# Performance work log

Hardware: AMD Instinct MI355X
Metric: run time of the kernel (lower is better)

Reference implementation:

```python
import jax, jax.numpy as jnp
import numpy as np

E = 8        # num_experts
K = 2        # top_k routing
D = 1024     # d_model
F = 4096     # expert hidden (ffn) dim
EPS = 1e-5


def _layernorm(h, g, b):
    # h: [E, T, C]; g, b: [E, C]
    mu = h.mean(axis=-1, keepdims=True)
    var = ((h - mu) ** 2).mean(axis=-1, keepdims=True)
    return (h - mu) * jax.lax.rsqrt(var + EPS) * g[:, None, :] + b[:, None, :]


def setup_inputs() -> dict:
    key = jax.random.key(0)
    ks = jax.random.split(key, 8)
    B, S = 2, 2048
    x = jax.random.normal(ks[0], (B, S, D), dtype=jnp.float32)
    Wr = jax.random.normal(ks[1], (D, E), dtype=jnp.float32) / np.sqrt(D)
    br = jnp.zeros((E,), dtype=jnp.float32)
    W1 = jax.random.normal(ks[2], (E, D, F), dtype=jnp.float32) / np.sqrt(D)
    b1 = jnp.zeros((E, F), dtype=jnp.float32)
    g1 = jnp.ones((E, F), dtype=jnp.float32)
    be1 = jnp.zeros((E, F), dtype=jnp.float32)
    W2 = jax.random.normal(ks[3], (E, F, D), dtype=jnp.float32) / np.sqrt(F)
    b2 = jnp.zeros((E, D), dtype=jnp.float32)
    g2 = jnp.ones((E, D), dtype=jnp.float32)
    be2 = jnp.zeros((E, D), dtype=jnp.float32)
    return {"x": x, "Wr": Wr, "br": br, "W1": W1, "b1": b1, "g1": g1,
            "be1": be1, "W2": W2, "b2": b2, "g2": g2, "be2": be2}


def reference(x, Wr, br, W1, b1, g1, be1, W2, b2, g2, be2):
    B, S, _ = x.shape
    xt = x.reshape(-1, D)                       # [T, D] token matrix
    # --- router + sampler: top-k softmax probs, renormalized over the k slots
    logits = xt @ Wr + br                       # [T, E]
    p = jax.nn.softmax(logits, axis=-1)
    probs, idx = jax.lax.top_k(p, K)            # [T, K]
    probs = probs / probs.sum(axis=-1, keepdims=True)
    # --- experts layer 1: Linear -> relu -> LayerNorm, per expert
    h = jnp.einsum('td,edf->etf', xt, W1) + b1[:, None, :]   # [E, T, F]
    h = _layernorm(jax.nn.relu(h), g1, be1)
    # --- experts layer 2: Linear -> relu -> LayerNorm
    y = jnp.einsum('etf,efd->etd', h, W2) + b2[:, None, :]   # [E, T, D]
    y = _layernorm(jax.nn.relu(y), g2, be2)
    # --- weighted scatter-combine: gate[t,e] = sum_k 1[idx[t,k]==e] * probs[t,k]
    gate = (jax.nn.one_hot(idx, E, dtype=x.dtype) * probs[..., None]).sum(axis=1)  # [T, E]
    out = jnp.einsum('te,etd->td', gate, y)     # index_add combine, dense form
    return out.reshape(B, S, D)
```

## Files before the change

kernel.cpp:

```cpp
#include <hip/hip_runtime.h>


#define E_N 8
#define TOPK 2
#define DM 1024
#define FF 4096
#define NTOK 4096
#define NA 8192
#define LN_EPS 1e-5f
#define NBX 128

typedef __attribute__((ext_vector_type(4))) float f32x4;
typedef __attribute__((ext_vector_type(8))) short short8;

__device__ __forceinline__ unsigned short f2bf(float f) {
    unsigned int u = __builtin_bit_cast(unsigned int, f);
    u = (u + 0x7FFFu + ((u >> 16) & 1u)) >> 16;
    return (unsigned short)u;
}
__device__ __forceinline__ float bf2f(unsigned short h) {
    unsigned int u = ((unsigned int)h) << 16;
    return __builtin_bit_cast(float, u);
}
__device__ __forceinline__ void unp(unsigned int u, float& lo, float& hi) {
    lo = bf2f((unsigned short)(u & 0xffffu));
    hi = bf2f((unsigned short)(u >> 16));
}
__device__ __forceinline__ unsigned int pk(float lo, float hi) {
    return (unsigned int)f2bf(lo) | ((unsigned int)f2bf(hi) << 16);
}

__device__ __forceinline__ void gload16(const unsigned short* g, unsigned short* lds) {
    __builtin_amdgcn_global_load_lds(
        (const __attribute__((address_space(1))) unsigned int*)g,
        (__attribute__((address_space(3))) unsigned int*)lds, 16, 0, 0);
}

__device__ __forceinline__ void transpose64(const float* __restrict__ s, int sld,
                                            unsigned short* __restrict__ d, int dld,
                                            float* tile) {
    int tid = threadIdx.x;
    int lr = tid >> 4, lc = (tid & 15) * 4;
#pragma unroll
    for (int p = 0; p < 4; p++) {
        int r = lr + p * 16;
        float4 v = *(const float4*)(s + (size_t)r * sld + lc);
        *(float4*)&tile[r * 64 + (lc ^ (((r >> 3) & 7) << 2))] = v;
    }
    __syncthreads();
    int a = tid & 7;
    int col = (tid >> 3) * 2;
    int cbase = (col & ~3) ^ (a << 2);
    int clo = col & 3;
    unsigned int o0[4], o1[4];
#pragma unroll
    for (int i = 0; i < 8; i += 2) {
        int r0 = 8 * a + i;
        float2 xy0 = *(const float2*)&tile[r0 * 64 + cbase + clo];
        float2 xy1 = *(const float2*)&tile[(r0 + 1) * 64 + cbase + clo];
        o0[i >> 1] = pk(xy0.x, xy1.x);
        o1[i >> 1] = pk(xy0.y, xy1.y);
    }
    *(uint4*)(d + (size_t)col * dld + 8 * a) = *(uint4*)o0;
    *(uint4*)(d + (size_t)(col + 1) * dld + 8 * a) = *(uint4*)o1;
}


__global__ __launch_bounds__(256) void k_prep(
        const float* __restrict__ W1, unsigned short* __restrict__ W1T,
        const float* __restrict__ x, const float* __restrict__ Wr,
        const float* __restrict__ br, unsigned short* __restrict__ xb,
        int* __restrict__ topk_idx, float* __restrict__ topk_p)
{
    __shared__ float tile[64 * 64];
    int z = blockIdx.z;
    int tid = threadIdx.x;

    if (z == 8) {
        int wv = tid >> 6, lane = tid & 63;
        int t = blockIdx.x * 4 + wv;
        const float* xr = x + (size_t)t * DM;
        unsigned short* xbr = xb + (size_t)t * DM;
        float a0=0,a1=0,a2=0,a3=0,a4=0,a5=0,a6=0,a7=0;
#pragma unroll
        for (int p = 0; p < 4; p++) {
            int d0 = p * 256 + lane * 4;
            float4 xv = *(const float4*)(xr + d0);
            uint2 pkd; pkd.x = pk(xv.x, xv.y); pkd.y = pk(xv.z, xv.w);
            *(uint2*)(xbr + d0) = pkd;
            float xs[4] = {xv.x, xv.y, xv.z, xv.w};
#pragma unroll
            for (int j = 0; j < 4; j++) {
                const float4* wp = (const float4*)(Wr + (d0 + j) * 8);
                float4 w0 = wp[0], w1 = wp[1];
                a0 += xs[j] * w0.x; a1 += xs[j] * w0.y; a2 += xs[j] * w0.z; a3 += xs[j] * w0.w;
                a4 += xs[j] * w1.x; a5 += xs[j] * w1.y; a6 += xs[j] * w1.z; a7 += xs[j] * w1.w;
            }
        }
#pragma unroll
        for (int off = 32; off; off >>= 1) {
            a0 += __shfl_xor(a0, off); a1 += __shfl_xor(a1, off);
            a2 += __shfl_xor(a2, off); a3 += __shfl_xor(a3, off);
            a4 += __shfl_xor(a4, off); a5 += __shfl_xor(a5, off);
            a6 += __shfl_xor(a6, off); a7 += __shfl_xor(a7, off);
        }
        if (lane == 0) {
            float l[8] = {a0 + br[0], a1 + br[1], a2 + br[2], a3 + br[3],
                          a4 + br[4], a5 + br[5], a6 + br[6], a7 + br[7]};
            int i0 = 0;
#pragma unroll
            for (int e = 1; e < 8; e++) if (l[e] > l[i0]) i0 = e;
            int i1 = (i0 == 0) ? 1 : 0;
#pragma unroll
            for (int e = 0; e < 8; e++) if (e != i0 && l[e] > l[i1]) i1 = e;
            float p1 = expf(l[i1] - l[i0]);
            float s = 1.0f + p1;
            topk_idx[2 * t]     = i0;
            topk_idx[2 * t + 1] = i1;
            topk_p[2 * t]       = 1.0f / s;
            topk_p[2 * t + 1]   = p1 / s;
        }
        return;
    }

    int bx = blockIdx.x & 63, by = blockIdx.x >> 6;
    transpose64(W1 + (size_t)z * DM * FF + (size_t)(by * 64) * FF + bx * 64, FF,
                W1T + (size_t)z * DM * FF + (size_t)(bx * 64) * DM + by * 64, DM,
                tile);
}


__global__ __launch_bounds__(256) void k_route2(const int* __restrict__ topk_idx,
        int* __restrict__ cnt, int* __restrict__ offs,
        int* __restrict__ assign_tok, int* __restrict__ assign_e,
        int* __restrict__ slot)
{
    __shared__ int h[8], base[8];
    int tid = threadIdx.x;
    if (tid < 8) h[tid] = 0;
    __syncthreads();
    int el[32];
#pragma unroll
    for (int i = 0; i < 32; i++) {
        int idx = tid * 32 + i;
        el[i] = topk_idx[idx];
        atomicAdd(&h[el[i]], 1);
    }
    __syncthreads();
    if (tid == 0) {
        int s = 0;
        for (int e = 0; e < E_N; e++) { offs[e] = s; cnt[e] = h[e]; base[e] = s; s += h[e]; }
        offs[E_N] = s;
    }
    __syncthreads();
    if (tid < 8) h[tid] = base[tid];
    __syncthreads();
#pragma unroll
    for (int i = 0; i < 32; i++) {
        int idx = tid * 32 + i;
        int e = el[i];
        int pos = atomicAdd(&h[e], 1);
        assign_tok[pos] = idx >> 1;
        assign_e[pos] = e;
        slot[idx] = pos;
    }
}


template<bool GATHER, bool EPI, bool TRANS>
__global__ __launch_bounds__(256, 4) void k_gemm(
    const unsigned short* __restrict__ A,
    const unsigned short* __restrict__ BT,
    const float* __restrict__ bias,
    unsigned short* __restrict__ C,
    const int* __restrict__ cnt, const int* __restrict__ offs,
    const int* __restrict__ gather_tok,
    const float* __restrict__ Wsrc, unsigned short* __restrict__ Wdst,
    int Kslice, int N, int ldA, int ldB, int GX, int KS, size_t slicePitch)
{
    __shared__ __align__(1024) char lds[32768];

    int bid = blockIdx.x;
    int e = bid & 7;
    int lb = bid >> 3;
    int M = cnt[e];
    if (M <= 0) return;
    int off_e = offs[e];
    int nrows = (M + 127) >> 7;
    int ntiles_g = nrows * GX * KS;
    int ntiles = ntiles_g + (TRANS ? 1024 : 0);

    int tid = threadIdx.x;
    int wv = tid >> 6, lane = tid & 63;
    int lr = lane & 15, hi = lane >> 4;
    int mW = (wv >> 1) * 64, nW = (wv & 1) * 64;
    int colsw = ((lane & 7) ^ (lane >> 3)) * 8;
    int l3 = lane >> 3;
    int nt = Kslice >> 6;

    for (int t = lb; t < ntiles; t += NBX) {
        if (TRANS && t >= ntiles_g) {
            int tt = t - ntiles_g;
            int bx = tt & 15, by = tt >> 4;
            __syncthreads();
            transpose64(Wsrc + (size_t)e * FF * DM + (size_t)(by * 64) * DM + bx * 64, DM,
                        Wdst + (size_t)e * DM * FF + (size_t)(bx * 64) * FF + by * 64, FF,
                        (float*)lds);
            continue;
        }

        int r = t % nrows;
        int q = t / nrows;
        int xn = q % GX;
        int ks = q / GX;
        int m0 = r * 128;
        int n0 = xn * 128;
        int kbase = ks * Kslice;

        const unsigned short* aptr[4];
        const unsigned short* bptr[4];
#pragma unroll
        for (int i = 0; i < 4; i++) {
            int j = wv * 4 + i;
            int rr = m0 + j * 8 + l3; rr = (rr < M) ? rr : (M - 1);
            size_t arow = GATHER ? (size_t)gather_tok[off_e + rr] : (size_t)(off_e + rr);
            aptr[i] = A + arow * (size_t)ldA + kbase + colsw;
            int rb = n0 + j * 8 + l3;
            bptr[i] = BT + ((size_t)e * N + rb) * (size_t)ldB + kbase + colsw;
        }

        f32x4 acc[4][4];
        f32x4 zz = {0.f, 0.f, 0.f, 0.f};
#pragma unroll
        for (int mi = 0; mi < 4; mi++)
#pragma unroll
            for (int ni = 0; ni < 4; ni++) acc[mi][ni] = zz;

        for (int kt = 0; kt < nt; ++kt) {
            __syncthreads();
#pragma unroll
            for (int i = 0; i < 4; i++) {
                gload16(aptr[i] + kt * 64, (unsigned short*)(lds + (wv * 4 + i) * 1024));
                gload16(bptr[i] + kt * 64, (unsigned short*)(lds + 16384 + (wv * 4 + i) * 1024));
            }
            __syncthreads();
#pragma unroll
            for (int kss = 0; kss < 2; kss++) {
                int cb = (kss * 64 + hi * 16) ^ ((lr & 7) << 4);
                short8 afr[4], bfr[4];
#pragma unroll
                for (int ni = 0; ni < 4; ni++)
                    bfr[ni] = *(const short8*)(lds + 16384 + (nW + ni * 16 + lr) * 128 + cb);
#pragma unroll
                for (int mi = 0; mi < 4; mi++)
                    afr[mi] = *(const short8*)(lds + (mW + mi * 16 + lr) * 128 + cb);
                __builtin_amdgcn_s_setprio(1);
#pragma unroll
                for (int mi = 0; mi < 4; mi++)
#pragma unroll
                    for (int ni = 0; ni < 4; ni++)
                        acc[mi][ni] = __builtin_amdgcn_mfma_f32_16x16x32_bf16(
                            afr[mi], bfr[ni], acc[mi][ni], 0, 0, 0);
                __builtin_amdgcn_s_setprio(0);
            }
        }

        unsigned short* Cs = C + ks * slicePitch;
        float bv[4] = {0.f, 0.f, 0.f, 0.f};
        if (EPI) {
#pragma unroll
            for (int ni = 0; ni < 4; ni++)
                bv[ni] = bias[(size_t)e * N + (n0 + nW + ni * 16 + lr)];
        }
#pragma unroll
        for (int mi = 0; mi < 4; mi++) {
            int mb = m0 + mW + mi * 16 + hi * 4;
#pragma unroll
            for (int rr = 0; rr < 4; rr++) {
                int m = mb + rr;
                if (m < M) {
                    unsigned short* crow = Cs + (size_t)(off_e + m) * N;
#pragma unroll
                    for (int ni = 0; ni < 4; ni++) {
                        float v = acc[mi][ni][rr];
                        if (EPI) v = fmaxf(v + bv[ni], 0.0f);
                        crow[n0 + nW + ni * 16 + lr] = f2bf(v);
                    }
                }
            }
        }
    }
}


__global__ __launch_bounds__(256) void k_ln1(unsigned short* __restrict__ H,
        const float* __restrict__ g, const float* __restrict__ b,
        const int* __restrict__ assign_e)
{
    size_t a = blockIdx.x;
    int e = assign_e[a];
    unsigned short* row = H + a * FF;
    int tid = threadIdx.x;
    uint4 u0 = *(const uint4*)(row + tid * 16);
    uint4 u1 = *(const uint4*)(row + tid * 16 + 8);
    float v[16];
    unp(u0.x, v[0], v[1]);  unp(u0.y, v[2], v[3]);
    unp(u0.z, v[4], v[5]);  unp(u0.w, v[6], v[7]);
    unp(u1.x, v[8], v[9]);  unp(u1.y, v[10], v[11]);
    unp(u1.z, v[12], v[13]); unp(u1.w, v[14], v[15]);
    float s = 0.f, q = 0.f;
#pragma unroll
    for (int i = 0; i < 16; i++) { s += v[i]; q += v[i] * v[i]; }
#pragma unroll
    for (int off = 32; off; off >>= 1) { s += __shfl_xor(s, off); q += __shfl_xor(q, off); }
    __shared__ float red[8];
    int wv = tid >> 6, lane = tid & 63;
    if (lane == 0) { red[wv * 2] = s; red[wv * 2 + 1] = q; }
    __syncthreads();
    s = red[0] + red[2] + red[4] + red[6];
    q = red[1] + red[3] + red[5] + red[7];
    float mu = s * (1.0f / FF);
    float var = q * (1.0f / FF) - mu * mu;
    float rstd = rsqrtf(var + LN_EPS);
    const float* gg = g + (size_t)e * FF + tid * 16;
    const float* bb = b + (size_t)e * FF + tid * 16;
    float4 G0 = *(const float4*)(gg);      float4 G1 = *(const float4*)(gg + 4);
    float4 G2 = *(const float4*)(gg + 8);  float4 G3 = *(const float4*)(gg + 12);
    float4 B0 = *(const float4*)(bb);      float4 B1 = *(const float4*)(bb + 4);
    float4 B2 = *(const float4*)(bb + 8);  float4 B3 = *(const float4*)(bb + 12);
    float gvv[16] = {G0.x,G0.y,G0.z,G0.w,G1.x,G1.y,G1.z,G1.w,G2.x,G2.y,G2.z,G2.w,G3.x,G3.y,G3.z,G3.w};
    float bvv[16] = {B0.x,B0.y,B0.z,B0.w,B1.x,B1.y,B1.z,B1.w,B2.x,B2.y,B2.z,B2.w,B3.x,B3.y,B3.z,B3.w};
#pragma unroll
    for (int i = 0; i < 16; i++) v[i] = (v[i] - mu) * rstd * gvv[i] + bvv[i];
    u0.x = pk(v[0], v[1]);  u0.y = pk(v[2], v[3]);
    u0.z = pk(v[4], v[5]);  u0.w = pk(v[6], v[7]);
    u1.x = pk(v[8], v[9]);  u1.y = pk(v[10], v[11]);
    u1.z = pk(v[12], v[13]); u1.w = pk(v[14], v[15]);
    *(uint4*)(row + tid * 16) = u0;
    *(uint4*)(row + tid * 16 + 8) = u1;
}


__global__ __launch_bounds__(256) void k_comb(const unsigned short* __restrict__ Yp,
        const float* __restrict__ g, const float* __restrict__ b2,
        const float* __restrict__ be,
        const int* __restrict__ slot, const float* __restrict__ topk_p,
        const int* __restrict__ assign_e, float* __restrict__ out)
{
    int t = blockIdx.x;
    int s0 = slot[2 * t], s1 = slot[2 * t + 1];
    float p0 = topk_p[2 * t], p1 = topk_p[2 * t + 1];
    int e0 = assign_e[s0], e1 = assign_e[s1];
    int tid = threadIdx.x;
    int d = tid * 4;
    const unsigned short* Y1 = Yp + (size_t)NA * DM;
    uint2 ua0 = *(const uint2*)(Yp + (size_t)s0 * DM + d);
    uint2 ua1 = *(const uint2*)(Y1 + (size_t)s0 * DM + d);
    uint2 ub0 = *(const uint2*)(Yp + (size_t)s1 * DM + d);
    uint2 ub1 = *(const uint2*)(Y1 + (size_t)s1 * DM + d);
    float4 bza = *(const float4*)(b2 + (size_t)e0 * DM + d);
    float4 bzb = *(const float4*)(b2 + (size_t)e1 * DM + d);
    float x0, x1, y0, y1;
    float va[4], vb[4];
    unp(ua0.x, x0, x1); unp(ua1.x, y0, y1);
    va[0] = fmaxf(x0 + y0 + bza.x, 0.f); va[1] = fmaxf(x1 + y1 + bza.y, 0.f);
    unp(ua0.y, x0, x1); unp(ua1.y, y0, y1);
    va[2] = fmaxf(x0 + y0 + bza.z, 0.f); va[3] = fmaxf(x1 + y1 + bza.w, 0.f);
    unp(ub0.x, x0, x1); unp(ub1.x, y0, y1);
    vb[0] = fmaxf(x0 + y0 + bzb.x, 0.f); vb[1] = fmaxf(x1 + y1 + bzb.y, 0.f);
    unp(ub0.y, x0, x1); unp(ub1.y, y0, y1);
    vb[2] = fmaxf(x0 + y0 + bzb.z, 0.f); vb[3] = fmaxf(x1 + y1 + bzb.w, 0.f);

    float sa = 0.f, qa = 0.f, sb = 0.f, qb = 0.f;
#pragma unroll
    for (int i = 0; i < 4; i++) {
        sa += va[i]; qa += va[i] * va[i];
        sb += vb[i]; qb += vb[i] * vb[i];
    }
#pragma unroll
    for (int off = 32; off; off >>= 1) {
        sa += __shfl_xor(sa, off); qa += __shfl_xor(qa, off);
        sb += __shfl_xor(sb, off); qb += __shfl_xor(qb, off);
    }
    __shared__ float red[16];
    int wv = tid >> 6, lane = tid & 63;
    if (lane == 0) { red[wv*4+0]=sa; red[wv*4+1]=qa; red[wv*4+2]=sb; red[wv*4+3]=qb; }
    __syncthreads();
    sa = red[0] + red[4] + red[8]  + red[12];
    qa = red[1] + red[5] + red[9]  + red[13];
    sb = red[2] + red[6] + red[10] + red[14];
    qb = red[3] + red[7] + red[11] + red[15];
    float mua = sa * (1.0f / DM), vara = qa * (1.0f / DM) - mua * mua;
    float ra = rsqrtf(vara + LN_EPS);
    float mub = sb * (1.0f / DM), varb = qb * (1.0f / DM) - mub * mub;
    float rb = rsqrtf(varb + LN_EPS);
    float4 ga  = *(const float4*)(g + (size_t)e0 * DM + d);
    float4 ba  = *(const float4*)(be + (size_t)e0 * DM + d);
    float4 gb4 = *(const float4*)(g + (size_t)e1 * DM + d);
    float4 bb4 = *(const float4*)(be + (size_t)e1 * DM + d);
    float4 o;
    o.x = p0 * ((va[0] - mua) * ra * ga.x + ba.x) + p1 * ((vb[0] - mub) * rb * gb4.x + bb4.x);
    o.y = p0 * ((va[1] - mua) * ra * ga.y + ba.y) + p1 * ((vb[1] - mub) * rb * gb4.y + bb4.y);
    o.z = p0 * ((va[2] - mua) * ra * ga.z + ba.z) + p1 * ((vb[2] - mub) * rb * gb4.z + bb4.z);
    o.w = p0 * ((va[3] - mua) * ra * ga.w + ba.w) + p1 * ((vb[3] - mub) * rb * gb4.w + bb4.w);
    *(float4*)(out + (size_t)t * DM + d) = o;
}


extern "C" void kernel_launch(void* const* d_in, const int* in_sizes, int n_in,
                              void* d_out, int out_size, void* d_ws, size_t ws_size,
                              hipStream_t stream) {
    const float* x   = (const float*)d_in[0];
    const float* Wr  = (const float*)d_in[1];
    const float* br  = (const float*)d_in[2];
    const float* W1  = (const float*)d_in[3];
    const float* b1  = (const float*)d_in[4];
    const float* g1  = (const float*)d_in[5];
    const float* be1 = (const float*)d_in[6];
    const float* W2  = (const float*)d_in[7];
    const float* b2  = (const float*)d_in[8];
    const float* g2  = (const float*)d_in[9];
    const float* be2 = (const float*)d_in[10];
    float* out = (float*)d_out;

    char* w = (char*)d_ws;
    int*   cnt        = (int*)(w);
    int*   offs       = (int*)(w + 128);
    int*   topk_idx   = (int*)(w + 512);
    float* topk_p     = (float*)(w + 512 + (32 << 10));
    int*   assign_tok = (int*)(w + 512 + (64 << 10));
    int*   assign_e   = (int*)(w + 512 + (96 << 10));
    int*   slot       = (int*)(w + 512 + (128 << 10));
    unsigned short* xb  = (unsigned short*)(w + ((size_t)1 << 20));
    unsigned short* W1T = (unsigned short*)(w + ((size_t)9 << 20));
    unsigned short* W2T = (unsigned short*)(w + ((size_t)73 << 20));
    unsigned short* Hb  = (unsigned short*)(w + ((size_t)137 << 20));
    unsigned short* Yp  = (unsigned short*)(w + ((size_t)201 << 20));

    k_prep<<<dim3(1024, 1, 9), 256, 0, stream>>>(
        W1, W1T, x, Wr, br, xb, topk_idx, topk_p);
    k_route2<<<1, 256, 0, stream>>>(topk_idx, cnt, offs, assign_tok, assign_e, slot);
    k_gemm<true, true, true><<<8 * NBX, 256, 0, stream>>>(
        xb, W1T, b1, Hb, cnt, offs, assign_tok, W2, W2T,
        DM, FF, DM, DM, 32, 1, 0);
    k_ln1<<<NA, 256, 0, stream>>>(Hb, g1, be1, assign_e);
    k_gemm<false, false, false><<<8 * NBX, 256, 0, stream>>>(
        Hb, W2T, nullptr, Yp, cnt, offs, nullptr, nullptr, nullptr,
        FF / 2, DM, FF, FF, 8, 2, (size_t)NA * DM);
    k_comb<<<NTOK, 256, 0, stream>>>(Yp, g2, b2, be2, slot, topk_p, assign_e, out);
}
```

Measured before the change: 335.1 us.

## Rewrite expert GEMMs as 256x256 8-wave tiles with 4-stage LDS pipeline

```diff
diff --git a/kernel.cpp b/kernel.cpp
--- a/kernel.cpp
+++ b/kernel.cpp
@@ -8,7 +8,6 @@
 #define NTOK 4096
 #define NA 8192
 #define LN_EPS 1e-5f
-#define NBX 128
 
 typedef __attribute__((ext_vector_type(4))) float f32x4;
 typedef __attribute__((ext_vector_type(8))) short short8;
@@ -30,7 +29,7 @@
     return (unsigned int)f2bf(lo) | ((unsigned int)f2bf(hi) << 16);
 }
 
-__device__ __forceinline__ void gload16(const unsigned short* g, unsigned short* lds) {
+__device__ __forceinline__ void gload16(const unsigned short* g, char* lds) {
     __builtin_amdgcn_global_load_lds(
         (const __attribute__((address_space(1))) unsigned int*)g,
         (__attribute__((address_space(3))) unsigned int*)lds, 16, 0, 0);
@@ -67,7 +66,8 @@
 
 
 __global__ __launch_bounds__(256) void k_prep(
-        const float* __restrict__ W1, unsigned short* __restrict__ W1T,
+        const float* __restrict__ W1, const float* __restrict__ W2,
+        unsigned short* __restrict__ W1T, unsigned short* __restrict__ W2T,
         const float* __restrict__ x, const float* __restrict__ Wr,
         const float* __restrict__ br, unsigned short* __restrict__ xb,
         int* __restrict__ topk_idx, float* __restrict__ topk_p)
@@ -76,7 +76,7 @@
     int z = blockIdx.z;
     int tid = threadIdx.x;
 
-    if (z == 8) {
+    if (z == 16) {
         int wv = tid >> 6, lane = tid & 63;
         int t = blockIdx.x * 4 + wv;
         const float* xr = x + (size_t)t * DM;
@@ -123,10 +123,18 @@
         return;
     }
 
-    int bx = blockIdx.x & 63, by = blockIdx.x >> 6;
-    transpose64(W1 + (size_t)z * DM * FF + (size_t)(by * 64) * FF + bx * 64, FF,
-                W1T + (size_t)z * DM * FF + (size_t)(bx * 64) * DM + by * 64, DM,
-                tile);
+    if (z < 8) {
+        int bx = blockIdx.x & 63, by = blockIdx.x >> 6;
+        transpose64(W1 + (size_t)z * DM * FF + (size_t)(by * 64) * FF + bx * 64, FF,
+                    W1T + (size_t)z * DM * FF + (size_t)(bx * 64) * DM + by * 64, DM,
+                    tile);
+    } else {
+        int e = z - 8;
+        int bx = blockIdx.x & 15, by = blockIdx.x >> 4;
+        transpose64(W2 + (size_t)e * FF * DM + (size_t)(by * 64) * DM + bx * 64, DM,
+                    W2T + (size_t)e * DM * FF + (size_t)(bx * 64) * FF + by * 64, FF,
+                    tile);
+    }
 }
 
 
@@ -167,18 +175,17 @@
 }
 
 
-template<bool GATHER, bool EPI, bool TRANS>
-__global__ __launch_bounds__(256, 4) void k_gemm(
+template<bool GATHER, bool EPI>
+__global__ __launch_bounds__(512, 2) void k_gemm8p(
     const unsigned short* __restrict__ A,
     const unsigned short* __restrict__ BT,
     const float* __restrict__ bias,
     unsigned short* __restrict__ C,
     const int* __restrict__ cnt, const int* __restrict__ offs,
     const int* __restrict__ gather_tok,
-    const float* __restrict__ Wsrc, unsigned short* __restrict__ Wdst,
     int Kslice, int N, int ldA, int ldB, int GX, int KS, size_t slicePitch)
 {
-    __shared__ __align__(1024) char lds[32768];
+    __shared__ __align__(1024) char lds[4][32768];
 
     int bid = blockIdx.x;
     int e = bid & 7;
@@ -186,95 +193,111 @@
     int M = cnt[e];
     if (M <= 0) return;
     int off_e = offs[e];
-    int nrows = (M + 127) >> 7;
-    int ntiles_g = nrows * GX * KS;
-    int ntiles = ntiles_g + (TRANS ? 1024 : 0);
+    int nrows = (M + 255) >> 8;
+    int ntiles = nrows * GX * KS;
 
     int tid = threadIdx.x;
     int wv = tid >> 6, lane = tid & 63;
     int lr = lane & 15, hi = lane >> 4;
-    int mW = (wv >> 1) * 64, nW = (wv & 1) * 64;
-    int colsw = ((lane & 7) ^ (lane >> 3)) * 8;
-    int l3 = lane >> 3;
-    int nt = Kslice >> 6;
-
-    for (int t = lb; t < ntiles; t += NBX) {
-        if (TRANS && t >= ntiles_g) {
-            int tt = t - ntiles_g;
-            int bx = tt & 15, by = tt >> 4;
-            __syncthreads();
-            transpose64(Wsrc + (size_t)e * FF * DM + (size_t)(by * 64) * DM + bx * 64, DM,
-                        Wdst + (size_t)e * DM * FF + (size_t)(bx * 64) * FF + by * 64, FF,
-                        (float*)lds);
-            continue;
-        }
-
+    int wr = wv >> 2, wc = wv & 3;
+    int ntk = Kslice >> 5;
+    int sr = lane >> 2;
+    int scol = ((lane & 3) ^ ((lane >> 3) & 3)) * 8;
+    int rsw = (lr >> 1) & 3;
+
+    for (int t = lb; t < ntiles; t += 32) {
         int r = t % nrows;
         int q = t / nrows;
         int xn = q % GX;
         int ks = q / GX;
-        int m0 = r * 128;
-        int n0 = xn * 128;
-        int kbase = ks * Kslice;
-
-        const unsigned short* aptr[4];
-        const unsigned short* bptr[4];
-#pragma unroll
-        for (int i = 0; i < 4; i++) {
-            int j = wv * 4 + i;
-            int rr = m0 + j * 8 + l3; rr = (rr < M) ? rr : (M - 1);
+        int m0 = r * 256, n0 = xn * 256, kbase = ks * Kslice;
+
+        const unsigned short* aSrc[2];
+        const unsigned short* bSrc[2];
+#pragma unroll
+        for (int i = 0; i < 2; i++) {
+            int u = wv * 2 + i;
+            int rr = m0 + u * 16 + sr; rr = (rr < M) ? rr : (M - 1);
             size_t arow = GATHER ? (size_t)gather_tok[off_e + rr] : (size_t)(off_e + rr);
-            aptr[i] = A + arow * (size_t)ldA + kbase + colsw;
-            int rb = n0 + j * 8 + l3;
-            bptr[i] = BT + ((size_t)e * N + rb) * (size_t)ldB + kbase + colsw;
-        }
-
-        f32x4 acc[4][4];
+            aSrc[i] = A + arow * (size_t)ldA + kbase + scol;
+            int nb = n0 + u * 16 + sr;
+            bSrc[i] = BT + ((size_t)e * N + nb) * (size_t)ldB + kbase + scol;
+        }
+
+        f32x4 acc[8][4];
         f32x4 zz = {0.f, 0.f, 0.f, 0.f};
 #pragma unroll
-        for (int mi = 0; mi < 4; mi++)
+        for (int mi = 0; mi < 8; mi++)
 #pragma unroll
             for (int ni = 0; ni < 4; ni++) acc[mi][ni] = zz;
 
-        for (int kt = 0; kt < nt; ++kt) {
-            __syncthreads();
-#pragma unroll
-            for (int i = 0; i < 4; i++) {
-                gload16(aptr[i] + kt * 64, (unsigned short*)(lds + (wv * 4 + i) * 1024));
-                gload16(bptr[i] + kt * 64, (unsigned short*)(lds + 16384 + (wv * 4 + i) * 1024));
+#pragma unroll
+        for (int tt = 0; tt < 4; tt++) {
+#pragma unroll
+            for (int i = 0; i < 2; i++) {
+                gload16(aSrc[i] + tt * 32, lds[tt] + (wv * 2 + i) * 1024);
+                gload16(bSrc[i] + tt * 32, lds[tt] + 16384 + (wv * 2 + i) * 1024);
             }
-            __syncthreads();
-#pragma unroll
-            for (int kss = 0; kss < 2; kss++) {
-                int cb = (kss * 64 + hi * 16) ^ ((lr & 7) << 4);
-                short8 afr[4], bfr[4];
-#pragma unroll
-                for (int ni = 0; ni < 4; ni++)
-                    bfr[ni] = *(const short8*)(lds + 16384 + (nW + ni * 16 + lr) * 128 + cb);
+        }
+        asm volatile("s_waitcnt vmcnt(12)" ::: "memory");
+        __builtin_amdgcn_s_barrier();
+
+        int niter = ntk >> 2;
+        for (int it = 0; it < niter; ++it) {
+            int k4 = it << 2;
+            short8 bfr[4];
+#pragma unroll
+            for (int p = 0; p < 8; p++) {
+                const int tj = p >> 1, mh = p & 1, sb = (tj + 3) & 3;
+                const char* cur = lds[tj];
+                short8 afr[4];
+                if (mh == 0) {
+#pragma unroll
+                    for (int ni = 0; ni < 4; ni++) {
+                        int row = wc * 64 + ni * 16 + lr;
+                        bfr[ni] = *(const short8*)(cur + 16384 + row * 64 + ((hi ^ rsw) << 4));
+                    }
+                }
+#pragma unroll
+                for (int mi = 0; mi < 4; mi++) {
+                    int row = wr * 128 + (mh * 4 + mi) * 16 + lr;
+                    afr[mi] = *(const short8*)(cur + row * 64 + ((hi ^ rsw) << 4));
+                }
+                int st = k4 + 3 + tj;
+                if (st >= 4) {
+                    int kof = ((st < ntk) ? st : (ntk - 1)) * 32;
+                    gload16(aSrc[mh] + kof, lds[sb] + (wv * 2 + mh) * 1024);
+                    gload16(bSrc[mh] + kof, lds[sb] + 16384 + (wv * 2 + mh) * 1024);
+                }
+                __builtin_amdgcn_s_barrier();
+                asm volatile("s_waitcnt lgkmcnt(0)" ::: "memory");
+                __builtin_amdgcn_sched_barrier(0);
+                __builtin_amdgcn_s_setprio(1);
 #pragma unroll
                 for (int mi = 0; mi < 4; mi++)
-                    afr[mi] = *(const short8*)(lds + (mW + mi * 16 + lr) * 128 + cb);
-                __builtin_amdgcn_s_setprio(1);
-#pragma unroll
-                for (int mi = 0; mi < 4; mi++)
 #pragma unroll
                     for (int ni = 0; ni < 4; ni++)
-                        acc[mi][ni] = __builtin_amdgcn_mfma_f32_16x16x32_bf16(
-                            afr[mi], bfr[ni], acc[mi][ni], 0, 0, 0);
+                        acc[mh * 4 + mi][ni] = __builtin_amdgcn_mfma_f32_16x16x32_bf16(
+                            afr[mi], bfr[ni], acc[mh * 4 + mi][ni], 0, 0, 0);
                 __builtin_amdgcn_s_setprio(0);
+                if (mh == 1)
+                    asm volatile("s_waitcnt vmcnt(8)" ::: "memory");
+                __builtin_amdgcn_s_barrier();
             }
         }
+        asm volatile("s_waitcnt vmcnt(0) lgkmcnt(0)" ::: "memory");
+        __builtin_amdgcn_s_barrier();
 
         unsigned short* Cs = C + ks * slicePitch;
         float bv[4] = {0.f, 0.f, 0.f, 0.f};
         if (EPI) {
 #pragma unroll
             for (int ni = 0; ni < 4; ni++)
-                bv[ni] = bias[(size_t)e * N + (n0 + nW + ni * 16 + lr)];
-        }
-#pragma unroll
-        for (int mi = 0; mi < 4; mi++) {
-            int mb = m0 + mW + mi * 16 + hi * 4;
+                bv[ni] = bias[(size_t)e * N + (n0 + wc * 64 + ni * 16 + lr)];
+        }
+#pragma unroll
+        for (int mi = 0; mi < 8; mi++) {
+            int mb = m0 + wr * 128 + mi * 16 + hi * 4;
 #pragma unroll
             for (int rr = 0; rr < 4; rr++) {
                 int m = mb + rr;
@@ -284,7 +307,7 @@
                     for (int ni = 0; ni < 4; ni++) {
                         float v = acc[mi][ni][rr];
                         if (EPI) v = fmaxf(v + bv[ni], 0.0f);
-                        crow[n0 + nW + ni * 16 + lr] = f2bf(v);
+                        crow[n0 + wc * 64 + ni * 16 + lr] = f2bf(v);
                     }
                 }
             }
@@ -437,15 +460,14 @@
     unsigned short* Hb  = (unsigned short*)(w + ((size_t)137 << 20));
     unsigned short* Yp  = (unsigned short*)(w + ((size_t)201 << 20));
 
-    k_prep<<<dim3(1024, 1, 9), 256, 0, stream>>>(
-        W1, W1T, x, Wr, br, xb, topk_idx, topk_p);
+    k_prep<<<dim3(1024, 1, 17), 256, 0, stream>>>(
+        W1, W2, W1T, W2T, x, Wr, br, xb, topk_idx, topk_p);
     k_route2<<<1, 256, 0, stream>>>(topk_idx, cnt, offs, assign_tok, assign_e, slot);
-    k_gemm<true, true, true><<<8 * NBX, 256, 0, stream>>>(
-        xb, W1T, b1, Hb, cnt, offs, assign_tok, W2, W2T,
-        DM, FF, DM, DM, 32, 1, 0);
+    k_gemm8p<true, true><<<256, 512, 0, stream>>>(
+        xb, W1T, b1, Hb, cnt, offs, assign_tok, DM, FF, DM, DM, 16, 1, 0);
     k_ln1<<<NA, 256, 0, stream>>>(Hb, g1, be1, assign_e);
-    k_gemm<false, false, false><<<8 * NBX, 256, 0, stream>>>(
-        Hb, W2T, nullptr, Yp, cnt, offs, nullptr, nullptr, nullptr,
-        FF / 2, DM, FF, FF, 8, 2, (size_t)NA * DM);
+    k_gemm8p<false, false><<<256, 512, 0, stream>>>(
+        Hb, W2T, nullptr, Yp, cnt, offs, nullptr, FF / 2, DM, FF, FF, 4, 2,
+        (size_t)NA * DM);
     k_comb<<<NTOK, 256, 0, stream>>>(Yp, g2, b2, be2, slot, topk_p, assign_e, out);
 }
```

Measured after the change: 354.4 us. +5.7%, slower.
